# Kernel optimization log

Measured on AMD Instinct MI355X. Metric: run time of the kernel, lower is better.

## Reference

```python
import jax, jax.numpy as jnp
import numpy as np
from jax import lax

TAU = 0.1
LAMBDA_ABCD = 0.5
NUM_ANCHORS = 256
THRESH = 0.6
NEG_INF = -1e30


def sample_features(feat, anchors):
    # feat: [B,C,H,W], anchors: [B,N,2] in [0,1] (u,v). Bilinear, align_corners=False, zeros padding.
    B, C, H, W = feat.shape
    g = anchors * 2.0 - 1.0
    x = ((g[..., 0] + 1.0) * W - 1.0) / 2.0  # [B,N] pixel coords
    y = ((g[..., 1] + 1.0) * H - 1.0) / 2.0
    x0 = jnp.floor(x).astype(jnp.int32); x1 = x0 + 1
    y0 = jnp.floor(y).astype(jnp.int32); y1 = y0 + 1
    wx1 = x - x0.astype(x.dtype); wx0 = 1.0 - wx1
    wy1 = y - y0.astype(y.dtype); wy0 = 1.0 - wy1
    flat = feat.reshape(B, C, H * W)

    def gather(xi, yi):
        valid = ((xi >= 0) & (xi < W) & (yi >= 0) & (yi < H)).astype(feat.dtype)
        idx = jnp.clip(yi, 0, H - 1) * W + jnp.clip(xi, 0, W - 1)  # [B,N]
        v = jnp.take_along_axis(flat, idx[:, None, :], axis=2)  # [B,C,N]
        return v * valid[:, None, :]

    out = (gather(x0, y0) * (wx0 * wy0)[:, None, :]
           + gather(x1, y0) * (wx1 * wy0)[:, None, :]
           + gather(x0, y1) * (wx0 * wy1)[:, None, :]
           + gather(x1, y1) * (wx1 * wy1)[:, None, :])
    return out.transpose(0, 2, 1)  # [B,N,C]


def layer_norm(x, gamma, beta, eps=1e-5):
    mu = x.mean(-1, keepdims=True)
    var = ((x - mu) ** 2).mean(-1, keepdims=True)
    return (x - mu) * lax.rsqrt(var + eps) * gamma + beta


def l2norm(x, eps=1e-12):
    n = jnp.sqrt(jnp.sum(x * x, -1, keepdims=True))
    return x / jnp.maximum(n, eps)


def conv2d(x, w, b, pad):
    y = lax.conv_general_dilated(x, w, (1, 1), pad,
                                 dimension_numbers=('NCHW', 'OIHW', 'NCHW'))
    return y + b[None, :, None, None]


def setup_inputs() -> dict:
    key = jax.random.key(0)
    ks = jax.random.split(key, 12)
    B, Ct, Cs, H, W, P = 16, 1024, 512, 64, 64, 256
    s = lambda k, shp, fan: jax.random.normal(k, shp, jnp.float32) * (1.0 / np.sqrt(fan))
    return {
        'teacher_feat': jax.random.normal(ks[0], (B, Ct, H, W), jnp.float32),
        'student_feat': jax.random.normal(ks[1], (B, Cs, H, W), jnp.float32),
        'conv1_w': s(ks[2], (Ct // 2, Ct, 3, 3), Ct * 9),
        'conv1_b': jnp.zeros((Ct // 2,), jnp.float32),
        'conv2_w': s(ks[3], (1, Ct // 2, 1, 1), Ct // 2),
        'conv2_b': jnp.zeros((1,), jnp.float32),
        't_w': s(ks[4], (Ct, P), Ct), 't_b': jnp.zeros((P,), jnp.float32),
        't_g': jnp.ones((P,), jnp.float32), 't_beta': jnp.zeros((P,), jnp.float32),
        's_w': s(ks[5], (Cs, P), Cs), 's_b': jnp.zeros((P,), jnp.float32),
        's_g': jnp.ones((P,), jnp.float32), 's_beta': jnp.zeros((P,), jnp.float32),
    }


def reference(teacher_feat, student_feat, conv1_w, conv1_b, conv2_w, conv2_b,
              t_w, t_b, t_g, t_beta, s_w, s_b, s_g, s_beta):
    B, Ct, H, W = teacher_feat.shape
    # learnable anchor generator
    h = jax.nn.relu(conv2d(teacher_feat, conv1_w, conv1_b, 'SAME'))
    heatmap = jax.nn.softplus(conv2d(h, conv2_w, conv2_b, 'SAME'))  # [B,1,H,W]
    prob = heatmap.reshape(B, -1)
    prob = prob / (prob.sum(1, keepdims=True) + 1e-6)
    # multinomial without replacement via Gumbel top-k (fixed key -> deterministic)
    u01 = jax.random.uniform(jax.random.key(42), prob.shape, jnp.float32, 1e-8, 1.0)
    gumbel = -jnp.log(-jnp.log(u01))
    idx = lax.top_k(jnp.log(prob + 1e-12) + gumbel, NUM_ANCHORS)[1]  # [B,N]
    ax = (idx % W).astype(jnp.float32) / W
    ay = (idx // W).astype(jnp.float32) / H
    anchors = jnp.stack([ax, ay], -1)  # [B,N,2]

    ft = sample_features(teacher_feat, anchors)  # [B,N,Ct]
    fs = sample_features(student_feat, anchors)  # [B,N,Cs]
    ft = l2norm(layer_norm(jnp.einsum('bnc,cp->bnp', ft, t_w) + t_b, t_g, t_beta))
    fs = l2norm(layer_norm(jnp.einsum('bnc,cp->bnp', fs, s_w) + s_b, s_g, s_beta))

    loss_gafd = jnp.mean((fs - lax.stop_gradient(ft)) ** 2)

    saliency = sample_features(heatmap, anchors)[..., 0]  # [B,N]
    bd = saliency > THRESH * saliency.max(1, keepdims=True)  # [B,N] bool
    non_bd = ~bd

    pos = jnp.sum(fs * ft, -1) / TAU                       # [B,N]
    neg = jnp.einsum('bnc,bmc->bnm', fs, fs) / TAU          # [B,N,N]
    neg = jnp.where(non_bd[:, None, :], neg, NEG_INF)
    logits = jnp.concatenate([pos[..., None], neg], -1)    # [B,N,N+1]
    row_loss = jax.nn.logsumexp(logits, -1) - pos          # [B,N]

    bd_f = bd.astype(jnp.float32)
    cnt = bd_f.sum(1)
    per_b = (row_loss * bd_f).sum(1) / jnp.maximum(cnt, 1.0)
    valid = ((cnt > 0) & (non_bd.sum(1) > 0)).astype(jnp.float32)
    vnum = valid.sum()
    loss_abcd = jnp.where(vnum > 0, (per_b * valid).sum() / jnp.maximum(vnum, 1.0), 0.0)

    total_loss = loss_gafd + LAMBDA_ABCD * loss_abcd
    return total_loss, loss_gafd, loss_abcd, heatmap
```

## Files before the change

### kernel.cpp

```cpp
#include <hip/hip_runtime.h>
#include <stdint.h>


typedef float f32x4 __attribute__((ext_vector_type(4)));
typedef short s16x8 __attribute__((ext_vector_type(8)));

__device__ __forceinline__ unsigned short f2bf(float f) {
  unsigned u = __float_as_uint(f);
  u += 0x7fffu + ((u >> 16) & 1u);
  return (unsigned short)(u >> 16);
}
__device__ __forceinline__ float bf2f(unsigned short h) {
  return __uint_as_float((unsigned)h << 16);
}

__device__ __forceinline__ void gld16(const void* g, void* l) {
  __builtin_amdgcn_global_load_lds(
      (const __attribute__((address_space(1))) void*)g,
      (__attribute__((address_space(3))) void*)l, 16, 0, 0);
}

__device__ __forceinline__ float block_sum(float v, float* l4) {
  for (int m = 32; m; m >>= 1) v += __shfl_xor(v, m, 64);
  int wid = threadIdx.x >> 6;
  if ((threadIdx.x & 63) == 0) l4[wid] = v;
  __syncthreads();
  float r = l4[0] + l4[1] + l4[2] + l4[3];
  __syncthreads();
  return r;
}

__global__ void k_pad_transpose(const float* __restrict__ teacher,
                                unsigned short* __restrict__ tpad) {
  __shared__ __align__(16) unsigned short lds[64 * 65];
  int bid = blockIdx.x;
  int cb = bid & 15, y = (bid >> 4) & 63, b = bid >> 10;
  int t = threadIdx.x;
#pragma unroll
  for (int it = 0; it < 16; ++it) {
    int idx = it * 256 + t;
    int cl = idx >> 6, x = idx & 63;
    float v = teacher[(size_t)(b * 1024 + cb * 64 + cl) * 4096 + y * 64 + x];
    lds[cl * 65 + x] = f2bf(v);
  }
  __syncthreads();
  size_t obase = ((size_t)(b * 66 + y + 1) * 66 + 1) * 1024 + cb * 64;
#pragma unroll
  for (int it = 0; it < 16; ++it) {
    int x = it * 4 + (t >> 6);
    int cl = t & 63;
    tpad[obase + (size_t)x * 1024 + cl] = lds[cl * 65 + x];
  }
  if (y == 0) {
    for (int idx = t; idx < 66 * 64; idx += 256) {
      int col = idx >> 6, cl = idx & 63;
      tpad[((size_t)(b * 66) * 66 + col) * 1024 + cb * 64 + cl] = 0;
    }
  }
  if (y == 63) {
    for (int idx = t; idx < 66 * 64; idx += 256) {
      int col = idx >> 6, cl = idx & 63;
      tpad[((size_t)(b * 66 + 65) * 66 + col) * 1024 + cb * 64 + cl] = 0;
    }
  }
  if (t < 128) {
    int col = (t >= 64) ? 65 : 0;
    int cl = t & 63;
    tpad[((size_t)(b * 66 + y + 1) * 66 + col) * 1024 + cb * 64 + cl] = 0;
  }
}

__global__ void k_wprep(const float* __restrict__ w1,
                        unsigned short* __restrict__ wt) {
  __shared__ float wl[9216];
  int co = blockIdx.x, t = threadIdx.x;
  const float* src = w1 + (size_t)co * 9216;
  for (int i = t; i < 9216; i += 256) wl[i] = src[i];
  __syncthreads();
  for (int i = t; i < 9216; i += 256) {
    int tap = i >> 10;
    int ci = i - (tap << 10);
    int kb = ci >> 6, kc = ci & 63;
    wt[(size_t)tap * 524288 + (size_t)kb * 32768 + co * 64 + kc] = f2bf(wl[ci * 9 + tap]);
  }
}

__global__ void k_wT(const float* __restrict__ w, unsigned short* __restrict__ wT,
                     int K) {
  int e = blockIdx.x * 256 + threadIdx.x;
  int p = e / K, k = e - p * K;
  wT[e] = f2bf(w[(size_t)k * 256 + p]);
}

#define STAGE_A(buf, ts, h) do {                                              \
    int tap_ = (ts) >> 4, kb_ = (ts) & 15;                                    \
    int ky_ = tap_ / 3, kx_ = tap_ - ky_ * 3;                                 \
    unsigned o_ = (unsigned)(((ky_ * 66 + kx_) << 10) + (kb_ << 6));          \
    gld16(tpad + aoff[(h) * 2 + 0] + o_,                                      \
          (char*)(As[buf] + (((h) * 128 + wid * 8) << 6)));                   \
    gld16(tpad + aoff[(h) * 2 + 1] + o_,                                      \
          (char*)(As[buf] + (((h) * 128 + 64 + wid * 8) << 6)));              \
  } while (0)

#define STAGE_B(buf, ts, h) do {                                              \
    int tap_ = (ts) >> 4, kb_ = (ts) & 15;                                    \
    unsigned o_ = (unsigned)((tap_ << 19) + (kb_ << 15));                     \
    gld16(wt + boff[(h) * 2 + 0] + o_,                                        \
          (char*)(Bs[buf] + (((h) * 128 + wid * 8) << 6)));                   \
    gld16(wt + boff[(h) * 2 + 1] + o_,                                        \
          (char*)(Bs[buf] + (((h) * 128 + 64 + wid * 8) << 6)));              \
  } while (0)

#define LDA8(AF, buf, i0)                                                     \
  _Pragma("unroll") for (int i_ = 0; i_ < 4; ++i_)                            \
  _Pragma("unroll") for (int s_ = 0; s_ < 2; ++s_)                            \
    AF[i_][s_] = *(const s16x8*)(const void*)(                                \
        &As[buf][(wm * 128 + ((i0) + i_) * 16 + l15) * 64 +                   \
                 ((s_ * 4 + quad) ^ sw7) * 8]);

#define LDB4(BF, buf, j0)                                                     \
  _Pragma("unroll") for (int j_ = 0; j_ < 2; ++j_)                            \
  _Pragma("unroll") for (int s_ = 0; s_ < 2; ++s_)                            \
    BF[j_][s_] = *(const s16x8*)(const void*)(                                \
        &Bs[buf][(wn * 64 + ((j0) + j_) * 16 + l15) * 64 +                    \
                 ((s_ * 4 + quad) ^ sw7) * 8]);

#define MFMA16(AF, BF, i0, j0)                                                \
  _Pragma("unroll") for (int i_ = 0; i_ < 4; ++i_)                            \
  _Pragma("unroll") for (int j_ = 0; j_ < 2; ++j_)                            \
  _Pragma("unroll") for (int s_ = 0; s_ < 2; ++s_)                            \
    acc[(i0) + i_][(j0) + j_] = __builtin_amdgcn_mfma_f32_16x16x32_bf16(      \
        AF[i_][s_], BF[j_][s_], acc[(i0) + i_][(j0) + j_], 0, 0, 0);

#define PHASE_MID()                                                           \
  __builtin_amdgcn_s_barrier();                                               \
  asm volatile("s_waitcnt lgkmcnt(0)" ::: "memory");                          \
  __builtin_amdgcn_sched_barrier(0);                                          \
  __builtin_amdgcn_s_setprio(1)

#define PHASE_END()                                                           \
  __builtin_amdgcn_s_setprio(0);                                              \
  __builtin_amdgcn_sched_barrier(0);                                          \
  __builtin_amdgcn_s_barrier()

#define PHASE_END_VM()                                                        \
  __builtin_amdgcn_s_setprio(0);                                              \
  __builtin_amdgcn_sched_barrier(0);                                          \
  asm volatile("s_waitcnt vmcnt(4)" ::: "memory");                            \
  __builtin_amdgcn_s_barrier()

__global__ __launch_bounds__(512, 2) void k_conv(
    const unsigned short* __restrict__ tpad, const unsigned short* __restrict__ wt,
    const float* __restrict__ b1, const float* __restrict__ w2,
    float* __restrict__ heat) {
  __shared__ __align__(16) unsigned short As[2][256 * 64];
  __shared__ __align__(16) unsigned short Bs[2][256 * 64];
  int bid = blockIdx.x;
  int swz = (bid & 7) * 64 + (bid >> 3);
  int nt = swz & 1, mt = swz >> 1;
  int m0 = mt * 256, n0 = nt * 256;
  int t = threadIdx.x, wid = t >> 6, lane = t & 63;
  int wm = wid >> 2, wn = wid & 3;
  int quad = lane >> 4, l15 = lane & 15;
  int sw7 = l15 & 7;

  int srcChunk = (t & 7) ^ ((t >> 3) & 7);
  unsigned aoff[4], boff[4];
#pragma unroll
  for (int v = 0; v < 4; ++v) {
    int row = (v >> 1) * 128 + (v & 1) * 64 + (t >> 3);
    int m = m0 + row;
    int b = m >> 12, y = (m >> 6) & 63, x = m & 63;
    aoff[v] = (unsigned)((((b * 66 + y) * 66 + x) << 10) + srcChunk * 8);
    boff[v] = (unsigned)(((n0 + row) << 6) + srcChunk * 8);
  }

  f32x4 acc[8][4];
  const f32x4 fz = {0.f, 0.f, 0.f, 0.f};
#pragma unroll
  for (int i = 0; i < 8; ++i)
#pragma unroll
    for (int j = 0; j < 4; ++j) acc[i][j] = fz;

  STAGE_B(0, 0, 0); STAGE_B(0, 0, 1);
  STAGE_A(0, 0, 0); STAGE_A(0, 0, 1);
  STAGE_B(1, 1, 0); STAGE_B(1, 1, 1);
  asm volatile("s_waitcnt vmcnt(4)" ::: "memory");
  __builtin_amdgcn_s_barrier();

  for (int it2 = 0; it2 < 72; ++it2) {
    int T0 = it2 * 2, T1 = T0 + 1;
    int tsN0 = (T0 + 2 <= 143) ? T0 + 2 : 143;
    int tsN1 = (T1 + 2 <= 143) ? T1 + 2 : 143;
    s16x8 af[4][2], bf01[2][2], bf23[2][2];
    LDA8(af, 0, 0);
    LDB4(bf01, 0, 0);
    STAGE_A(1, T1, 0);
    PHASE_MID();
    MFMA16(af, bf01, 0, 0);
    PHASE_END();

    LDB4(bf23, 0, 2);
    STAGE_A(1, T1, 1);
    PHASE_MID();
    MFMA16(af, bf23, 0, 2);
    PHASE_END();

    LDA8(af, 0, 4);
    STAGE_B(0, tsN0, 0);
    PHASE_MID();
    MFMA16(af, bf01, 4, 0);
    PHASE_END();

    STAGE_B(0, tsN0, 1);
    PHASE_MID();
    MFMA16(af, bf23, 4, 2);
    PHASE_END_VM();

    LDA8(af, 1, 0);
    LDB4(bf01, 1, 0);
    STAGE_A(0, tsN0, 0);
    PHASE_MID();
    MFMA16(af, bf01, 0, 0);
    PHASE_END();

    LDB4(bf23, 1, 2);
    STAGE_A(0, tsN0, 1);
    PHASE_MID();
    MFMA16(af, bf23, 0, 2);
    PHASE_END();

    LDA8(af, 1, 4);
    STAGE_B(1, tsN1, 0);
    PHASE_MID();
    MFMA16(af, bf01, 4, 0);
    PHASE_END();

    STAGE_B(1, tsN1, 1);
    PHASE_MID();
    MFMA16(af, bf23, 4, 2);
    PHASE_END_VM();
  }

  float w2v[4], b1v[4];
#pragma unroll
  for (int j = 0; j < 4; ++j) {
    int co = n0 + wn * 64 + j * 16 + l15;
    w2v[j] = w2[co];
    b1v[j] = b1[co];
  }
#pragma unroll
  for (int i = 0; i < 8; ++i) {
#pragma unroll
    for (int r = 0; r < 4; ++r) {
      float part = 0.f;
#pragma unroll
      for (int j = 0; j < 4; ++j) {
        float v = acc[i][j][r] + b1v[j];
        v = fmaxf(v, 0.f);
        part += v * w2v[j];
      }
#pragma unroll
      for (int msk = 1; msk < 16; msk <<= 1) part += __shfl_xor(part, msk, 64);
      if (l15 == 0) atomicAdd(&heat[m0 + wm * 128 + i * 16 + quad * 4 + r], part);
    }
  }
}

__device__ __forceinline__ unsigned rotl32(unsigned x, int d) {
  return (x << d) | (x >> (32 - d));
}
__device__ unsigned threefry_bits(unsigned lo) {
  const unsigned k0 = 0u, k1 = 42u;
  const unsigned k2 = 0x1BD11BDAu ^ k0 ^ k1;
  unsigned x0 = 0u + k0, x1 = lo + k1;
#define TF_R4(a, bq, c, d)                                \
  x0 += x1; x1 = rotl32(x1, a); x1 ^= x0;                 \
  x0 += x1; x1 = rotl32(x1, bq); x1 ^= x0;                \
  x0 += x1; x1 = rotl32(x1, c); x1 ^= x0;                 \
  x0 += x1; x1 = rotl32(x1, d); x1 ^= x0;
  TF_R4(13, 15, 26, 6)  x0 += k1; x1 += k2 + 1u;
  TF_R4(17, 29, 16, 24) x0 += k2; x1 += k0 + 2u;
  TF_R4(13, 15, 26, 6)  x0 += k0; x1 += k1 + 3u;
  TF_R4(17, 29, 16, 24) x0 += k1; x1 += k2 + 4u;
  TF_R4(13, 15, 26, 6)  x0 += k2; x1 += k0 + 5u;
#undef TF_R4
  return x0 ^ x1;
}

__global__ void k_heat2score(const float* __restrict__ heat, const float* __restrict__ b2p,
                             float* __restrict__ out_hm, float* __restrict__ hm,
                             float* __restrict__ scores) {
  __shared__ float l4[4];
  int b = blockIdx.x, t = threadIdx.x;
  float b2 = b2p[0];
  float hv[16];
  float lsum = 0.f;
#pragma unroll
  for (int j = 0; j < 16; ++j) {
    int e = j * 256 + t;
    float x = heat[b * 4096 + e] + b2;
    float sp = fmaxf(x, 0.f) + log1pf(expf(-fabsf(x)));
    hv[j] = sp;
    lsum += sp;
  }
  float S = block_sum(lsum, l4);
  float denom = S + 1e-6f;
#pragma unroll
  for (int j = 0; j < 16; ++j) {
    int e = j * 256 + t;
    float sp = hv[j];
    out_hm[b * 4096 + e] = sp;
    hm[b * 4096 + e] = sp;
    float lp = logf(sp / denom + 1e-12f);
    unsigned bits = threefry_bits((unsigned)(b * 4096 + e));
    float u01 = __uint_as_float((bits >> 9) | 0x3f800000u) - 1.0f;
    float u = fmaxf(1e-8f, u01 * (1.0f - 1e-8f) + 1e-8f);
    float gum = -logf(-logf(u));
    scores[b * 4096 + e] = lp + gum;
  }
}

__global__ void k_topk(const float* __restrict__ scores, int* __restrict__ idx_sel) {
  __shared__ unsigned keys[4096];
  __shared__ unsigned hist[256];
  __shared__ unsigned suf[256];
  __shared__ unsigned sel[2];
  __shared__ int wpos;
  int b = blockIdx.x, t = threadIdx.x;
#pragma unroll
  for (int j = 0; j < 16; ++j) {
    unsigned u = __float_as_uint(scores[b * 4096 + j * 256 + t]);
    u = (u >> 31) ? ~u : (u | 0x80000000u);
    keys[j * 256 + t] = u;
  }
  if (t == 0) wpos = 0;
  unsigned prefix = 0, hmask = 0, r = 256;
  for (int pass = 0; pass < 4; ++pass) {
    int shift = 24 - 8 * pass;
    hist[t] = 0;
    __syncthreads();
#pragma unroll
    for (int j = 0; j < 16; ++j) {
      unsigned u = keys[j * 256 + t];
      if ((u & hmask) == prefix) atomicAdd(&hist[(u >> shift) & 255u], 1u);
    }
    __syncthreads();
    suf[t] = hist[t];
    __syncthreads();
    for (int off = 1; off < 256; off <<= 1) {
      unsigned v = (t + off < 256) ? suf[t + off] : 0u;
      __syncthreads();
      suf[t] += v;
      __syncthreads();
    }
    unsigned above = (t < 255) ? suf[t + 1] : 0u;
    if (suf[t] >= r && above < r) {
      sel[0] = (unsigned)t;
      sel[1] = above;
    }
    __syncthreads();
    prefix |= sel[0] << shift;
    hmask |= 0xFFu << shift;
    r -= sel[1];
    __syncthreads();
  }
#pragma unroll
  for (int j = 0; j < 16; ++j) {
    int e = j * 256 + t;
    if (keys[e] > prefix) {
      int s = atomicAdd(&wpos, 1);
      idx_sel[b * 256 + s] = e;
    }
  }
  __syncthreads();
#pragma unroll
  for (int j = 0; j < 16; ++j) {
    int e = j * 256 + t;
    if (keys[e] == prefix) {
      int s = atomicAdd(&wpos, 1);
      if (s < 256) idx_sel[b * 256 + s] = e;
    }
  }
}

__global__ void k_gather_t(const unsigned short* __restrict__ tpad,
                           const int* __restrict__ idx_sel,
                           unsigned short* __restrict__ ftb) {
  int bn = blockIdx.x;
  int b = bn >> 8;
  int idx = idx_sel[bn];
  int px = idx & 63, py = idx >> 6;
  const unsigned short* base = tpad + ((size_t)(b * 66 + py) * 66 + px) * 1024;
  for (int c = threadIdx.x; c < 1024; c += 256) {
    float v = bf2f(base[c]) + bf2f(base[c + 1024]) +
              bf2f(base[c + 66 * 1024]) + bf2f(base[c + 67 * 1024]);
    ftb[(size_t)bn * 1024 + c] = f2bf(0.25f * v);
  }
}

__global__ void k_gather_s(const float* __restrict__ student,
                           const int* __restrict__ idx_sel,
                           unsigned short* __restrict__ fsbT) {
  __shared__ float plane[4096];
  int blk = blockIdx.x;
  int b = blk >> 9, c = blk & 511;
  int t = threadIdx.x;
  const float4* g4 = (const float4*)(student + ((size_t)b * 512 + c) * 4096);
  float4* p4 = (float4*)plane;
  for (int i = t; i < 1024; i += 256) p4[i] = g4[i];
  __syncthreads();
  int idx = idx_sel[b * 256 + t];
  int px = idx & 63, py = idx >> 6;
  float v = 0.f;
  if (py > 0) {
    if (px > 0) v += plane[(py - 1) * 64 + px - 1];
    v += plane[(py - 1) * 64 + px];
  }
  if (px > 0) v += plane[py * 64 + px - 1];
  v += plane[py * 64 + px];
  fsbT[((size_t)b * 512 + c) * 256 + t] = f2bf(0.25f * v);
}

__global__ void k_fsb_tr(const unsigned short* __restrict__ fsbT,
                         unsigned short* __restrict__ fsb) {
  __shared__ unsigned short tile[64][65];
  int blk = blockIdx.x;
  int b = blk >> 5, ct = (blk >> 2) & 7, nt = blk & 3;
  int t = threadIdx.x;
#pragma unroll
  for (int it = 0; it < 16; ++it) {
    int e = it * 256 + t;
    int cl = e >> 6, n = e & 63;
    tile[cl][n] = fsbT[((size_t)(b * 512 + ct * 64 + cl)) * 256 + nt * 64 + n];
  }
  __syncthreads();
#pragma unroll
  for (int it = 0; it < 16; ++it) {
    int e = it * 256 + t;
    int n = e >> 6, cl = e & 63;
    fsb[((size_t)(b * 256 + nt * 64 + n)) * 512 + ct * 64 + cl] = tile[cl][n];
  }
}

__global__ __launch_bounds__(256) void k_proj(
    const unsigned short* __restrict__ A, const unsigned short* __restrict__ Wt,
    int K, float* __restrict__ outp) {
  __shared__ __align__(16) unsigned short As[128 * 64];
  __shared__ __align__(16) unsigned short Bs[128 * 64];
  int bid = blockIdx.x;
  int nt = bid & 1, mt = bid >> 1;
  int m0 = mt * 128, n0 = nt * 128;
  int t = threadIdx.x, wid = t >> 6, lane = t & 63;
  int wm = wid & 1, wn = wid >> 1;
  int quad = lane >> 4, l15 = lane & 15;

  f32x4 acc[4][4];
  const f32x4 fz = {0.f, 0.f, 0.f, 0.f};
#pragma unroll
  for (int i = 0; i < 4; ++i)
#pragma unroll
    for (int j = 0; j < 4; ++j) acc[i][j] = fz;

  int row4[4];
#pragma unroll
  for (int jj = 0; jj < 4; ++jj) row4[jj] = (wid * 4 + jj) * 8 + (lane >> 3);
  int kcol = (lane & 7) * 8;

  int nkb = K >> 6;
  for (int kb = 0; kb < nkb; ++kb) {
#pragma unroll
    for (int jj = 0; jj < 4; ++jj) {
      gld16(A + (size_t)(m0 + row4[jj]) * K + kb * 64 + kcol,
            (char*)As + (wid * 4 + jj) * 1024);
      gld16(Wt + (size_t)(n0 + row4[jj]) * K + kb * 64 + kcol,
            (char*)Bs + (wid * 4 + jj) * 1024);
    }
    __syncthreads();
#pragma unroll
    for (int s = 0; s < 2; ++s) {
      s16x8 af[4], bf[4];
#pragma unroll
      for (int i = 0; i < 4; ++i) {
        af[i] = *(const s16x8*)(const void*)(As + (wm * 64 + i * 16 + l15) * 64 + s * 32 + quad * 8);
        bf[i] = *(const s16x8*)(const void*)(Bs + (wn * 64 + i * 16 + l15) * 64 + s * 32 + quad * 8);
      }
#pragma unroll
      for (int i = 0; i < 4; ++i)
#pragma unroll
        for (int j = 0; j < 4; ++j)
          acc[i][j] = __builtin_amdgcn_mfma_f32_16x16x32_bf16(af[i], bf[j], acc[i][j], 0, 0, 0);
    }
    __syncthreads();
  }
#pragma unroll
  for (int i = 0; i < 4; ++i)
#pragma unroll
    for (int j = 0; j < 4; ++j)
#pragma unroll
      for (int r = 0; r < 4; ++r) {
        int m = m0 + wm * 64 + i * 16 + quad * 4 + r;
        int p = n0 + wn * 64 + j * 16 + l15;
        outp[(size_t)m * 256 + p] = acc[i][j][r];
      }
}

__global__ void k_ln(const float* __restrict__ projp, const float* __restrict__ bias,
                     const float* __restrict__ g, const float* __restrict__ beta,
                     float* __restrict__ outf, unsigned short* __restrict__ outb) {
  __shared__ float l4[4];
  int row = blockIdx.x, t = threadIdx.x;
  float x = projp[(size_t)row * 256 + t] + bias[t];
  float s1 = block_sum(x, l4);
  float mu = s1 * (1.f / 256.f);
  float d = x - mu;
  float s2 = block_sum(d * d, l4);
  float rstd = rsqrtf(s2 * (1.f / 256.f) + 1e-5f);
  float xn = d * rstd * g[t] + beta[t];
  float ss = block_sum(xn * xn, l4);
  float o = xn / fmaxf(sqrtf(ss), 1e-12f);
  outf[(size_t)row * 256 + t] = o;
  if (outb) outb[(size_t)row * 256 + t] = f2bf(o);
}

__global__ void k_sal(const float* __restrict__ hm, const int* __restrict__ idx_sel,
                      int* __restrict__ bd, int* __restrict__ cnt, int* __restrict__ nbc) {
  __shared__ float l4[4];
  int b = blockIdx.x, t = threadIdx.x;
  int idx = idx_sel[b * 256 + t];
  int px = idx & 63, py = idx >> 6;
  const float* hb = hm + b * 4096;
  float v = 0.f;
  if (py > 0) {
    if (px > 0) v += hb[(py - 1) * 64 + px - 1];
    v += hb[(py - 1) * 64 + px];
  }
  if (px > 0) v += hb[py * 64 + px - 1];
  v += hb[py * 64 + px];
  float sal = 0.25f * v;
  float mx = sal;
  for (int m = 32; m; m >>= 1) mx = fmaxf(mx, __shfl_xor(mx, m, 64));
  if ((t & 63) == 0) l4[t >> 6] = mx;
  __syncthreads();
  mx = fmaxf(fmaxf(l4[0], l4[1]), fmaxf(l4[2], l4[3]));
  __syncthreads();
  int bdv = sal > 0.6f * mx ? 1 : 0;
  bd[b * 256 + t] = bdv;
  float c = block_sum((float)bdv, l4);
  if (t == 0) {
    cnt[b] = (int)c;
    nbc[b] = 256 - (int)c;
  }
}

__global__ void k_pos_gafd(const float* __restrict__ fsn, const float* __restrict__ ftn,
                           float* __restrict__ pos, float* __restrict__ gsum) {
  __shared__ float l4[4];
  int row = blockIdx.x, t = threadIdx.x;
  float a = fsn[(size_t)row * 256 + t];
  float bt = ftn[(size_t)row * 256 + t];
  float sdot = block_sum(a * bt, l4);
  if (t == 0) pos[row] = sdot * 10.f;
  float d = a - bt;
  float ssq = block_sum(d * d, l4);
  if (t == 0) atomicAdd(gsum, ssq);
}

__global__ __launch_bounds__(256) void k_abcd_rows(
    const unsigned short* __restrict__ fsnb, const int* __restrict__ bd,
    const float* __restrict__ pos, float* __restrict__ rowloss) {
  __shared__ __align__(16) unsigned short Ab[64 * 64];
  __shared__ __align__(16) unsigned short Bb[256 * 64];
  __shared__ float mrg[64][4][2];
  int b = blockIdx.x >> 2, nb = blockIdx.x & 3;
  int n0 = nb * 64;
  int t = threadIdx.x, w = t >> 6, lane = t & 63, quad = lane >> 4, l15 = lane & 15;
  f32x4 acc[4][4];
  const f32x4 fz = {0.f, 0.f, 0.f, 0.f};
#pragma unroll
  for (int i = 0; i < 4; ++i)
#pragma unroll
    for (int j = 0; j < 4; ++j) acc[i][j] = fz;
  const unsigned short* fb = fsnb + (size_t)b * 256 * 256;

  for (int kc = 0; kc < 4; ++kc) {
    {
      int r = t >> 2, cc = (t & 3) * 16;
      const uint4* s = (const uint4*)(const void*)(fb + (size_t)(n0 + r) * 256 + kc * 64 + cc);
      *(uint4*)(void*)(Ab + r * 64 + cc) = s[0];
      *(uint4*)(void*)(Ab + r * 64 + cc + 8) = s[1];
    }
#pragma unroll
    for (int it = 0; it < 4; ++it) {
      int m = it * 64 + (t >> 2), cc = (t & 3) * 16;
      const uint4* s = (const uint4*)(const void*)(fb + (size_t)m * 256 + kc * 64 + cc);
      *(uint4*)(void*)(Bb + m * 64 + cc) = s[0];
      *(uint4*)(void*)(Bb + m * 64 + cc + 8) = s[1];
    }
    __syncthreads();
#pragma unroll
    for (int s = 0; s < 2; ++s) {
      s16x8 af[4], bf[4];
#pragma unroll
      for (int i = 0; i < 4; ++i) {
        af[i] = *(const s16x8*)(const void*)(Ab + (i * 16 + l15) * 64 + s * 32 + quad * 8);
        bf[i] = *(const s16x8*)(const void*)(Bb + (w * 64 + i * 16 + l15) * 64 + s * 32 + quad * 8);
      }
#pragma unroll
      for (int i = 0; i < 4; ++i)
#pragma unroll
        for (int j = 0; j < 4; ++j)
          acc[i][j] = __builtin_amdgcn_mfma_f32_16x16x32_bf16(af[i], bf[j], acc[i][j], 0, 0, 0);
    }
    __syncthreads();
  }

  int nbmask[4];
#pragma unroll
  for (int j = 0; j < 4; ++j) nbmask[j] = bd[b * 256 + w * 64 + j * 16 + l15];
#pragma unroll
  for (int i = 0; i < 4; ++i) {
#pragma unroll
    for (int r = 0; r < 4; ++r) {
      float mxv = -1e30f, se = 0.f;
#pragma unroll
      for (int j = 0; j < 4; ++j) {
        float v = nbmask[j] ? -1e30f : (acc[i][j][r] / 0.1f);
        if (v > mxv) {
          se = se * expf(mxv - v) + 1.f;
          mxv = v;
        } else {
          se += expf(v - mxv);
        }
      }
#pragma unroll
      for (int msk = 1; msk < 16; msk <<= 1) {
        float omx = __shfl_xor(mxv, msk, 64);
        float ose = __shfl_xor(se, msk, 64);
        float nm = fmaxf(mxv, omx);
        se = se * expf(mxv - nm) + ose * expf(omx - nm);
        mxv = nm;
      }
      if (l15 == 0) {
        mrg[i * 16 + quad * 4 + r][w][0] = mxv;
        mrg[i * 16 + quad * 4 + r][w][1] = se;
      }
    }
  }
  __syncthreads();
  if (t < 64) {
    float MX = -1e30f, SE = 0.f;
    for (int ww = 0; ww < 4; ++ww) {
      float omx = mrg[t][ww][0], ose = mrg[t][ww][1];
      float nm = fmaxf(MX, omx);
      SE = SE * expf(MX - nm) + ose * expf(omx - nm);
      MX = nm;
    }
    float p = pos[b * 256 + n0 + t];
    float nm = fmaxf(MX, p);
    float se2 = SE * expf(MX - nm) + expf(p - nm);
    rowloss[b * 256 + n0 + t] = nm + logf(se2) - p;
  }
}

__global__ void k_final(const float* __restrict__ gsum, const float* __restrict__ rowloss,
                        const int* __restrict__ bd, const int* __restrict__ cnt,
                        const int* __restrict__ nbc, float* __restrict__ out) {
  __shared__ float l4[4];
  int t = threadIdx.x;
  float abcd_acc = 0.f, vnum = 0.f;
  for (int b = 0; b < 16; ++b) {
    float c = bd[b * 256 + t] ? rowloss[b * 256 + t] : 0.f;
    float s = block_sum(c, l4);
    if (t == 0) {
      float cb = (float)cnt[b];
      float per = s / fmaxf(cb, 1.f);
      if (cnt[b] > 0 && nbc[b] > 0) {
        abcd_acc += per;
        vnum += 1.f;
      }
    }
  }
  if (t == 0) {
    float gafd = gsum[0] / 1048576.f;
    float abcd = vnum > 0.f ? abcd_acc / fmaxf(vnum, 1.f) : 0.f;
    out[0] = gafd + 0.5f * abcd;
    out[1] = gafd;
    out[2] = abcd;
  }
}

static constexpr size_t OFF_TPAD = 0;
static constexpr size_t TPAD_BYTES = (size_t)16 * 66 * 66 * 1024 * 2;
static constexpr size_t OFF_WT = OFF_TPAD + TPAD_BYTES;
static constexpr size_t WT_BYTES = (size_t)9 * 16 * 512 * 64 * 2;
static constexpr size_t OFF_HEAT = OFF_WT + WT_BYTES;
static constexpr size_t OFF_GSUM = OFF_HEAT + 262144;
static constexpr size_t OFF_HM = OFF_GSUM + 256;
static constexpr size_t OFF_SC = OFF_HM + 262144;
static constexpr size_t OFF_IDX = OFF_SC + 262144;
static constexpr size_t OFF_FTB = OFF_IDX + 16384;
static constexpr size_t OFF_FSB = OFF_FTB + (size_t)4096 * 1024 * 2;
static constexpr size_t OFF_FSBT = OFF_FSB + (size_t)4096 * 512 * 2;
static constexpr size_t OFF_WTT = OFF_FSBT + (size_t)4096 * 512 * 2;
static constexpr size_t OFF_WTS = OFF_WTT + (size_t)256 * 1024 * 2;
static constexpr size_t OFF_PRT = OFF_WTS + (size_t)256 * 512 * 2;
static constexpr size_t OFF_PRS = OFF_PRT + (size_t)4096 * 256 * 4;
static constexpr size_t OFF_FTN = OFF_PRS + (size_t)4096 * 256 * 4;
static constexpr size_t OFF_FSN = OFF_FTN + (size_t)4096 * 256 * 4;
static constexpr size_t OFF_FSNB = OFF_FSN + (size_t)4096 * 256 * 4;
static constexpr size_t OFF_POS = OFF_FSNB + (size_t)4096 * 256 * 2;
static constexpr size_t OFF_BD = OFF_POS + 16384;
static constexpr size_t OFF_CNT = OFF_BD + 16384;
static constexpr size_t OFF_NBC = OFF_CNT + 64;
static constexpr size_t OFF_RL = OFF_NBC + 64;

extern "C" void kernel_launch(void* const* d_in, const int* in_sizes, int n_in,
                              void* d_out, int out_size, void* d_ws, size_t ws_size,
                              hipStream_t stream) {
  const float* teacher = (const float*)d_in[0];
  const float* student = (const float*)d_in[1];
  const float* w1 = (const float*)d_in[2];
  const float* b1 = (const float*)d_in[3];
  const float* w2 = (const float*)d_in[4];
  const float* b2 = (const float*)d_in[5];
  const float* t_w = (const float*)d_in[6];
  const float* t_b = (const float*)d_in[7];
  const float* t_g = (const float*)d_in[8];
  const float* t_be = (const float*)d_in[9];
  const float* s_w = (const float*)d_in[10];
  const float* s_b = (const float*)d_in[11];
  const float* s_g = (const float*)d_in[12];
  const float* s_be = (const float*)d_in[13];
  float* out = (float*)d_out;

  char* ws = (char*)d_ws;
  unsigned short* tpad = (unsigned short*)(ws + OFF_TPAD);
  unsigned short* wt = (unsigned short*)(ws + OFF_WT);
  float* heat = (float*)(ws + OFF_HEAT);
  float* gsum = (float*)(ws + OFF_GSUM);
  float* hm = (float*)(ws + OFF_HM);
  float* scores = (float*)(ws + OFF_SC);
  int* idx_sel = (int*)(ws + OFF_IDX);
  unsigned short* ftb = (unsigned short*)(ws + OFF_FTB);
  unsigned short* fsb = (unsigned short*)(ws + OFF_FSB);
  unsigned short* fsbT = (unsigned short*)(ws + OFF_FSBT);
  unsigned short* wTt = (unsigned short*)(ws + OFF_WTT);
  unsigned short* wTs = (unsigned short*)(ws + OFF_WTS);
  float* projt = (float*)(ws + OFF_PRT);
  float* projs = (float*)(ws + OFF_PRS);
  float* ftn = (float*)(ws + OFF_FTN);
  float* fsn = (float*)(ws + OFF_FSN);
  unsigned short* fsnb = (unsigned short*)(ws + OFF_FSNB);
  float* pos = (float*)(ws + OFF_POS);
  int* bd = (int*)(ws + OFF_BD);
  int* cnt = (int*)(ws + OFF_CNT);
  int* nbc = (int*)(ws + OFF_NBC);
  float* rowloss = (float*)(ws + OFF_RL);

  hipMemsetAsync(ws + OFF_HEAT, 0, 262144 + 256, stream);

  k_pad_transpose<<<16384, 256, 0, stream>>>(teacher, tpad);
  k_wprep<<<512, 256, 0, stream>>>(w1, wt);
  k_wT<<<1024, 256, 0, stream>>>(t_w, wTt, 1024);
  k_wT<<<512, 256, 0, stream>>>(s_w, wTs, 512);
  k_conv<<<512, 512, 0, stream>>>(tpad, wt, b1, w2, heat);
  k_heat2score<<<16, 256, 0, stream>>>(heat, b2, out + 3, hm, scores);
  k_topk<<<16, 256, 0, stream>>>(scores, idx_sel);
  k_gather_t<<<4096, 256, 0, stream>>>(tpad, idx_sel, ftb);
  k_gather_s<<<8192, 256, 0, stream>>>(student, idx_sel, fsbT);
  k_fsb_tr<<<512, 256, 0, stream>>>(fsbT, fsb);
  k_proj<<<64, 256, 0, stream>>>(ftb, wTt, 1024, projt);
  k_proj<<<64, 256, 0, stream>>>(fsb, wTs, 512, projs);
  k_ln<<<4096, 256, 0, stream>>>(projt, t_b, t_g, t_be, ftn, (unsigned short*)nullptr);
  k_ln<<<4096, 256, 0, stream>>>(projs, s_b, s_g, s_be, fsn, fsnb);
  k_sal<<<16, 256, 0, stream>>>(hm, idx_sel, bd, cnt, nbc);
  k_pos_gafd<<<4096, 256, 0, stream>>>(fsn, ftn, pos, gsum);
  k_abcd_rows<<<64, 256, 0, stream>>>(fsnb, bd, pos, rowloss);
  k_final<<<1, 256, 0, stream>>>(gsum, rowloss, bd, cnt, nbc, out);
}
```

Measured before the change: 1.194 ms.

## Fuse small kernels, vectorize transpose/gather, and reorder conv LDS loads

Several kernels are merged: the three weight-prep kernels become one launch, score/topk/saliency become one per-batch kernel that keeps the heatmap in LDS, the two projection GEMMs share one launch, and the student layernorm is fused with the pos/GAFD reduction. The pad-transpose and teacher gather now use 16-byte vector loads and stores. In the conv main loop, LDS fragment loads are issued earlier so they overlap with the preceding MFMAs. Together these cut launch overhead and intermediate global round-trips, at the cost of more LDS use and register pressure in the fused kernels.

```diff
diff --git a/kernel.cpp b/kernel.cpp
--- a/kernel.cpp
+++ b/kernel.cpp
@@ -37,19 +37,25 @@
   int cb = bid & 15, y = (bid >> 4) & 63, b = bid >> 10;
   int t = threadIdx.x;
 #pragma unroll
-  for (int it = 0; it < 16; ++it) {
+  for (int it = 0; it < 4; ++it) {
     int idx = it * 256 + t;
-    int cl = idx >> 6, x = idx & 63;
-    float v = teacher[(size_t)(b * 1024 + cb * 64 + cl) * 4096 + y * 64 + x];
-    lds[cl * 65 + x] = f2bf(v);
+    int cl = idx >> 4, x4 = (idx & 15) * 4;
+    float4 v = *(const float4*)&teacher[(size_t)(b * 1024 + cb * 64 + cl) * 4096 + y * 64 + x4];
+    lds[cl * 65 + x4 + 0] = f2bf(v.x);
+    lds[cl * 65 + x4 + 1] = f2bf(v.y);
+    lds[cl * 65 + x4 + 2] = f2bf(v.z);
+    lds[cl * 65 + x4 + 3] = f2bf(v.w);
   }
   __syncthreads();
   size_t obase = ((size_t)(b * 66 + y + 1) * 66 + 1) * 1024 + cb * 64;
 #pragma unroll
-  for (int it = 0; it < 16; ++it) {
-    int x = it * 4 + (t >> 6);
-    int cl = t & 63;
-    tpad[obase + (size_t)x * 1024 + cl] = lds[cl * 65 + x];
+  for (int it = 0; it < 2; ++it) {
+    int wi = it * 256 + t;
+    int x = wi >> 3, c0 = (wi & 7) * 8;
+    s16x8 v;
+#pragma unroll
+    for (int k2 = 0; k2 < 8; ++k2) v[k2] = (short)lds[(c0 + k2) * 65 + x];
+    *(s16x8*)(void*)&tpad[obase + (size_t)x * 1024 + c0] = v;
   }
   if (y == 0) {
     for (int idx = t; idx < 66 * 64; idx += 256) {
@@ -70,26 +76,32 @@
   }
 }
 
-__global__ void k_wprep(const float* __restrict__ w1,
-                        unsigned short* __restrict__ wt) {
-  __shared__ float wl[9216];
-  int co = blockIdx.x, t = threadIdx.x;
-  const float* src = w1 + (size_t)co * 9216;
-  for (int i = t; i < 9216; i += 256) wl[i] = src[i];
-  __syncthreads();
-  for (int i = t; i < 9216; i += 256) {
-    int tap = i >> 10;
-    int ci = i - (tap << 10);
-    int kb = ci >> 6, kc = ci & 63;
-    wt[(size_t)tap * 524288 + (size_t)kb * 32768 + co * 64 + kc] = f2bf(wl[ci * 9 + tap]);
-  }
-}
-
-__global__ void k_wT(const float* __restrict__ w, unsigned short* __restrict__ wT,
-                     int K) {
-  int e = blockIdx.x * 256 + threadIdx.x;
-  int p = e / K, k = e - p * K;
-  wT[e] = f2bf(w[(size_t)k * 256 + p]);
+__global__ void k_wprep_all(const float* __restrict__ w1,
+                            unsigned short* __restrict__ wt,
+                            const float* __restrict__ tw, unsigned short* __restrict__ wTt,
+                            const float* __restrict__ sw, unsigned short* __restrict__ wTs) {
+  int blk = blockIdx.x, t = threadIdx.x;
+  if (blk < 512) {
+    __shared__ float wl[9216];
+    int co = blk;
+    const float* src = w1 + (size_t)co * 9216;
+    for (int i = t; i < 9216; i += 256) wl[i] = src[i];
+    __syncthreads();
+    for (int i = t; i < 9216; i += 256) {
+      int tap = i >> 10;
+      int ci = i - (tap << 10);
+      int kb = ci >> 6, kc = ci & 63;
+      wt[(size_t)tap * 524288 + (size_t)kb * 32768 + co * 64 + kc] = f2bf(wl[ci * 9 + tap]);
+    }
+  } else if (blk < 1536) {
+    int e = (blk - 512) * 256 + t;
+    int p = e >> 10, k = e & 1023;
+    wTt[e] = f2bf(tw[(size_t)k * 256 + p]);
+  } else {
+    int e = (blk - 1536) * 256 + t;
+    int p = e >> 9, k = e & 511;
+    wTs[e] = f2bf(sw[(size_t)k * 256 + p]);
+  }
 }
 
 #define STAGE_A(buf, ts, h) do {                                              \
@@ -189,54 +201,54 @@
   __builtin_amdgcn_s_barrier();
 
   for (int it2 = 0; it2 < 72; ++it2) {
-    int T0 = it2 * 2, T1 = T0 + 1;
-    int tsN0 = (T0 + 2 <= 143) ? T0 + 2 : 143;
-    int tsN1 = (T1 + 2 <= 143) ? T1 + 2 : 143;
+    int T1 = it2 * 2 + 1;
+    int tsA = (T1 + 1 <= 143) ? T1 + 1 : 143;
+    int tsB = (T1 + 2 <= 143) ? T1 + 2 : 143;
     s16x8 af[4][2], bf01[2][2], bf23[2][2];
     LDA8(af, 0, 0);
     LDB4(bf01, 0, 0);
     STAGE_A(1, T1, 0);
     PHASE_MID();
     MFMA16(af, bf01, 0, 0);
+    LDB4(bf23, 0, 2);
     PHASE_END();
 
-    LDB4(bf23, 0, 2);
     STAGE_A(1, T1, 1);
     PHASE_MID();
     MFMA16(af, bf23, 0, 2);
+    LDA8(af, 0, 4);
     PHASE_END();
 
-    LDA8(af, 0, 4);
-    STAGE_B(0, tsN0, 0);
+    STAGE_B(0, tsA, 0);
     PHASE_MID();
     MFMA16(af, bf01, 4, 0);
     PHASE_END();
 
-    STAGE_B(0, tsN0, 1);
+    STAGE_B(0, tsA, 1);
     PHASE_MID();
     MFMA16(af, bf23, 4, 2);
     PHASE_END_VM();
 
     LDA8(af, 1, 0);
     LDB4(bf01, 1, 0);
-    STAGE_A(0, tsN0, 0);
+    STAGE_A(0, tsA, 0);
     PHASE_MID();
     MFMA16(af, bf01, 0, 0);
+    LDB4(bf23, 1, 2);
     PHASE_END();
 
-    LDB4(bf23, 1, 2);
-    STAGE_A(0, tsN0, 1);
+    STAGE_A(0, tsA, 1);
     PHASE_MID();
     MFMA16(af, bf23, 0, 2);
+    LDA8(af, 1, 4);
     PHASE_END();
 
-    LDA8(af, 1, 4);
-    STAGE_B(1, tsN1, 0);
+    STAGE_B(1, tsB, 0);
     PHASE_MID();
     MFMA16(af, bf01, 4, 0);
     PHASE_END();
 
-    STAGE_B(1, tsN1, 1);
+    STAGE_B(1, tsB, 1);
     PHASE_MID();
     MFMA16(af, bf23, 4, 2);
     PHASE_END_VM();
@@ -288,20 +300,29 @@
   return x0 ^ x1;
 }
 
-__global__ void k_heat2score(const float* __restrict__ heat, const float* __restrict__ b2p,
-                             float* __restrict__ out_hm, float* __restrict__ hm,
-                             float* __restrict__ scores) {
+__global__ void k_score_topk_sal(const float* __restrict__ heat,
+                                 const float* __restrict__ b2p,
+                                 float* __restrict__ out_hm,
+                                 int* __restrict__ idx_sel,
+                                 int* __restrict__ bd, int* __restrict__ cnt,
+                                 int* __restrict__ nbc) {
+  __shared__ float hmp[4096];
+  __shared__ unsigned keys[4096];
+  __shared__ unsigned hist[256];
+  __shared__ unsigned suf[256];
+  __shared__ unsigned sel[2];
+  __shared__ int wpos;
+  __shared__ int idxl[256];
   __shared__ float l4[4];
   int b = blockIdx.x, t = threadIdx.x;
   float b2 = b2p[0];
-  float hv[16];
   float lsum = 0.f;
 #pragma unroll
   for (int j = 0; j < 16; ++j) {
     int e = j * 256 + t;
     float x = heat[b * 4096 + e] + b2;
     float sp = fmaxf(x, 0.f) + log1pf(expf(-fabsf(x)));
-    hv[j] = sp;
+    hmp[e] = sp;
     lsum += sp;
   }
   float S = block_sum(lsum, l4);
@@ -309,30 +330,17 @@
 #pragma unroll
   for (int j = 0; j < 16; ++j) {
     int e = j * 256 + t;
-    float sp = hv[j];
+    float sp = hmp[e];
     out_hm[b * 4096 + e] = sp;
-    hm[b * 4096 + e] = sp;
     float lp = logf(sp / denom + 1e-12f);
     unsigned bits = threefry_bits((unsigned)(b * 4096 + e));
     float u01 = __uint_as_float((bits >> 9) | 0x3f800000u) - 1.0f;
     float u = fmaxf(1e-8f, u01 * (1.0f - 1e-8f) + 1e-8f);
     float gum = -logf(-logf(u));
-    scores[b * 4096 + e] = lp + gum;
-  }
-}
-
-__global__ void k_topk(const float* __restrict__ scores, int* __restrict__ idx_sel) {
-  __shared__ unsigned keys[4096];
-  __shared__ unsigned hist[256];
-  __shared__ unsigned suf[256];
-  __shared__ unsigned sel[2];
-  __shared__ int wpos;
-  int b = blockIdx.x, t = threadIdx.x;
-#pragma unroll
-  for (int j = 0; j < 16; ++j) {
-    unsigned u = __float_as_uint(scores[b * 4096 + j * 256 + t]);
-    u = (u >> 31) ? ~u : (u | 0x80000000u);
-    keys[j * 256 + t] = u;
+    float sc = lp + gum;
+    unsigned uu = __float_as_uint(sc);
+    uu = (uu >> 31) ? ~uu : (uu | 0x80000000u);
+    keys[e] = uu;
   }
   if (t == 0) wpos = 0;
   unsigned prefix = 0, hmask = 0, r = 256;
@@ -371,6 +379,7 @@
     if (keys[e] > prefix) {
       int s = atomicAdd(&wpos, 1);
       idx_sel[b * 256 + s] = e;
+      idxl[s] = e;
     }
   }
   __syncthreads();
@@ -379,24 +388,60 @@
     int e = j * 256 + t;
     if (keys[e] == prefix) {
       int s = atomicAdd(&wpos, 1);
-      if (s < 256) idx_sel[b * 256 + s] = e;
-    }
+      if (s < 256) {
+        idx_sel[b * 256 + s] = e;
+        idxl[s] = e;
+      }
+    }
+  }
+  __syncthreads();
+  int idx = idxl[t];
+  int px = idx & 63, py = idx >> 6;
+  float v = 0.f;
+  if (py > 0) {
+    if (px > 0) v += hmp[(py - 1) * 64 + px - 1];
+    v += hmp[(py - 1) * 64 + px];
+  }
+  if (px > 0) v += hmp[py * 64 + px - 1];
+  v += hmp[py * 64 + px];
+  float sal = 0.25f * v;
+  float mx = sal;
+  for (int m = 32; m; m >>= 1) mx = fmaxf(mx, __shfl_xor(mx, m, 64));
+  if ((t & 63) == 0) l4[t >> 6] = mx;
+  __syncthreads();
+  mx = fmaxf(fmaxf(l4[0], l4[1]), fmaxf(l4[2], l4[3]));
+  __syncthreads();
+  int bdv = sal > 0.6f * mx ? 1 : 0;
+  bd[b * 256 + t] = bdv;
+  float c = block_sum((float)bdv, l4);
+  if (t == 0) {
+    cnt[b] = (int)c;
+    nbc[b] = 256 - (int)c;
   }
 }
 
 __global__ void k_gather_t(const unsigned short* __restrict__ tpad,
                            const int* __restrict__ idx_sel,
                            unsigned short* __restrict__ ftb) {
-  int bn = blockIdx.x;
+  int t = threadIdx.x;
+  int bn = blockIdx.x * 2 + (t >> 7);
+  int tt = t & 127;
   int b = bn >> 8;
   int idx = idx_sel[bn];
   int px = idx & 63, py = idx >> 6;
-  const unsigned short* base = tpad + ((size_t)(b * 66 + py) * 66 + px) * 1024;
-  for (int c = threadIdx.x; c < 1024; c += 256) {
-    float v = bf2f(base[c]) + bf2f(base[c + 1024]) +
-              bf2f(base[c + 66 * 1024]) + bf2f(base[c + 67 * 1024]);
-    ftb[(size_t)bn * 1024 + c] = f2bf(0.25f * v);
-  }
+  const unsigned short* base = tpad + ((size_t)(b * 66 + py) * 66 + px) * 1024 + tt * 8;
+  s16x8 r0 = *(const s16x8*)(const void*)(base);
+  s16x8 r1 = *(const s16x8*)(const void*)(base + 1024);
+  s16x8 r2 = *(const s16x8*)(const void*)(base + 66 * 1024);
+  s16x8 r3 = *(const s16x8*)(const void*)(base + 67 * 1024);
+  s16x8 o;
+#pragma unroll
+  for (int k = 0; k < 8; ++k) {
+    float v = bf2f((unsigned short)r0[k]) + bf2f((unsigned short)r1[k]) +
+              bf2f((unsigned short)r2[k]) + bf2f((unsigned short)r3[k]);
+    o[k] = (short)f2bf(0.25f * v);
+  }
+  *(s16x8*)(void*)&ftb[(size_t)bn * 1024 + tt * 8] = o;
 }
 
 __global__ void k_gather_s(const float* __restrict__ student,
@@ -443,12 +488,19 @@
   }
 }
 
-__global__ __launch_bounds__(256) void k_proj(
-    const unsigned short* __restrict__ A, const unsigned short* __restrict__ Wt,
-    int K, float* __restrict__ outp) {
-  __shared__ __align__(16) unsigned short As[128 * 64];
-  __shared__ __align__(16) unsigned short Bs[128 * 64];
-  int bid = blockIdx.x;
+__global__ __launch_bounds__(256) void k_proj_both(
+    const unsigned short* __restrict__ At, const unsigned short* __restrict__ Wtt,
+    const unsigned short* __restrict__ Asrc, const unsigned short* __restrict__ Wts,
+    float* __restrict__ outt, float* __restrict__ outs) {
+  __shared__ __align__(16) unsigned short Al[128 * 64];
+  __shared__ __align__(16) unsigned short Bl[128 * 64];
+  int g = blockIdx.x;
+  const unsigned short* A;
+  const unsigned short* Wt;
+  float* outp;
+  int K, bid;
+  if (g < 64) { A = At; Wt = Wtt; outp = outt; K = 1024; bid = g; }
+  else        { A = Asrc; Wt = Wts; outp = outs; K = 512; bid = g - 64; }
   int nt = bid & 1, mt = bid >> 1;
   int m0 = mt * 128, n0 = nt * 128;
   int t = threadIdx.x, wid = t >> 6, lane = t & 63;
@@ -472,9 +524,9 @@
 #pragma unroll
     for (int jj = 0; jj < 4; ++jj) {
       gld16(A + (size_t)(m0 + row4[jj]) * K + kb * 64 + kcol,
-            (char*)As + (wid * 4 + jj) * 1024);
+            (char*)Al + (wid * 4 + jj) * 1024);
       gld16(Wt + (size_t)(n0 + row4[jj]) * K + kb * 64 + kcol,
-            (char*)Bs + (wid * 4 + jj) * 1024);
+            (char*)Bl + (wid * 4 + jj) * 1024);
     }
     __syncthreads();
 #pragma unroll
@@ -482,8 +534,8 @@
       s16x8 af[4], bf[4];
 #pragma unroll
       for (int i = 0; i < 4; ++i) {
-        af[i] = *(const s16x8*)(const void*)(As + (wm * 64 + i * 16 + l15) * 64 + s * 32 + quad * 8);
-        bf[i] = *(const s16x8*)(const void*)(Bs + (wn * 64 + i * 16 + l15) * 64 + s * 32 + quad * 8);
+        af[i] = *(const s16x8*)(const void*)(Al + (wm * 64 + i * 16 + l15) * 64 + s * 32 + quad * 8);
+        bf[i] = *(const s16x8*)(const void*)(Bl + (wn * 64 + i * 16 + l15) * 64 + s * 32 + quad * 8);
       }
 #pragma unroll
       for (int i = 0; i < 4; ++i)
@@ -507,7 +559,7 @@
 
 __global__ void k_ln(const float* __restrict__ projp, const float* __restrict__ bias,
                      const float* __restrict__ g, const float* __restrict__ beta,
-                     float* __restrict__ outf, unsigned short* __restrict__ outb) {
+                     float* __restrict__ outf) {
   __shared__ float l4[4];
   int row = blockIdx.x, t = threadIdx.x;
   float x = projp[(size_t)row * 256 + t] + bias[t];
@@ -520,49 +572,31 @@
   float ss = block_sum(xn * xn, l4);
   float o = xn / fmaxf(sqrtf(ss), 1e-12f);
   outf[(size_t)row * 256 + t] = o;
-  if (outb) outb[(size_t)row * 256 + t] = f2bf(o);
-}
-
-__global__ void k_sal(const float* __restrict__ hm, const int* __restrict__ idx_sel,
-                      int* __restrict__ bd, int* __restrict__ cnt, int* __restrict__ nbc) {
-  __shared__ float l4[4];
-  int b = blockIdx.x, t = threadIdx.x;
-  int idx = idx_sel[b * 256 + t];
-  int px = idx & 63, py = idx >> 6;
-  const float* hb = hm + b * 4096;
-  float v = 0.f;
-  if (py > 0) {
-    if (px > 0) v += hb[(py - 1) * 64 + px - 1];
-    v += hb[(py - 1) * 64 + px];
-  }
-  if (px > 0) v += hb[py * 64 + px - 1];
-  v += hb[py * 64 + px];
-  float sal = 0.25f * v;
-  float mx = sal;
-  for (int m = 32; m; m >>= 1) mx = fmaxf(mx, __shfl_xor(mx, m, 64));
-  if ((t & 63) == 0) l4[t >> 6] = mx;
-  __syncthreads();
-  mx = fmaxf(fmaxf(l4[0], l4[1]), fmaxf(l4[2], l4[3]));
-  __syncthreads();
-  int bdv = sal > 0.6f * mx ? 1 : 0;
-  bd[b * 256 + t] = bdv;
-  float c = block_sum((float)bdv, l4);
-  if (t == 0) {
-    cnt[b] = (int)c;
-    nbc[b] = 256 - (int)c;
-  }
-}
-
-__global__ void k_pos_gafd(const float* __restrict__ fsn, const float* __restrict__ ftn,
+}
+
+__global__ void k_ln_s_pos(const float* __restrict__ projp, const float* __restrict__ bias,
+                           const float* __restrict__ g, const float* __restrict__ beta,
+                           const float* __restrict__ ftn,
+                           float* __restrict__ outf, unsigned short* __restrict__ outb,
                            float* __restrict__ pos, float* __restrict__ gsum) {
   __shared__ float l4[4];
   int row = blockIdx.x, t = threadIdx.x;
-  float a = fsn[(size_t)row * 256 + t];
+  float x = projp[(size_t)row * 256 + t] + bias[t];
+  float s1 = block_sum(x, l4);
+  float mu = s1 * (1.f / 256.f);
+  float d = x - mu;
+  float s2 = block_sum(d * d, l4);
+  float rstd = rsqrtf(s2 * (1.f / 256.f) + 1e-5f);
+  float xn = d * rstd * g[t] + beta[t];
+  float ss = block_sum(xn * xn, l4);
+  float o = xn / fmaxf(sqrtf(ss), 1e-12f);
+  outf[(size_t)row * 256 + t] = o;
+  outb[(size_t)row * 256 + t] = f2bf(o);
   float bt = ftn[(size_t)row * 256 + t];
-  float sdot = block_sum(a * bt, l4);
+  float sdot = block_sum(o * bt, l4);
   if (t == 0) pos[row] = sdot * 10.f;
-  float d = a - bt;
-  float ssq = block_sum(d * d, l4);
+  float dd = o - bt;
+  float ssq = block_sum(dd * dd, l4);
   if (t == 0) atomicAdd(gsum, ssq);
 }
 
@@ -739,8 +773,6 @@
   unsigned short* wt = (unsigned short*)(ws + OFF_WT);
   float* heat = (float*)(ws + OFF_HEAT);
   float* gsum = (float*)(ws + OFF_GSUM);
-  float* hm = (float*)(ws + OFF_HM);
-  float* scores = (float*)(ws + OFF_SC);
   int* idx_sel = (int*)(ws + OFF_IDX);
   unsigned short* ftb = (unsigned short*)(ws + OFF_FTB);
   unsigned short* fsb = (unsigned short*)(ws + OFF_FSB);
@@ -761,21 +793,15 @@
   hipMemsetAsync(ws + OFF_HEAT, 0, 262144 + 256, stream);
 
   k_pad_transpose<<<16384, 256, 0, stream>>>(teacher, tpad);
-  k_wprep<<<512, 256, 0, stream>>>(w1, wt);
-  k_wT<<<1024, 256, 0, stream>>>(t_w, wTt, 1024);
-  k_wT<<<512, 256, 0, stream>>>(s_w, wTs, 512);
+  k_wprep_all<<<2048, 256, 0, stream>>>(w1, wt, t_w, wTt, s_w, wTs);
   k_conv<<<512, 512, 0, stream>>>(tpad, wt, b1, w2, heat);
-  k_heat2score<<<16, 256, 0, stream>>>(heat, b2, out + 3, hm, scores);
-  k_topk<<<16, 256, 0, stream>>>(scores, idx_sel);
-  k_gather_t<<<4096, 256, 0, stream>>>(tpad, idx_sel, ftb);
+  k_score_topk_sal<<<16, 256, 0, stream>>>(heat, b2, out + 3, idx_sel, bd, cnt, nbc);
+  k_gather_t<<<2048, 256, 0, stream>>>(tpad, idx_sel, ftb);
   k_gather_s<<<8192, 256, 0, stream>>>(student, idx_sel, fsbT);
   k_fsb_tr<<<512, 256, 0, stream>>>(fsbT, fsb);
-  k_proj<<<64, 256, 0, stream>>>(ftb, wTt, 1024, projt);
-  k_proj<<<64, 256, 0, stream>>>(fsb, wTs, 512, projs);
-  k_ln<<<4096, 256, 0, stream>>>(projt, t_b, t_g, t_be, ftn, (unsigned short*)nullptr);
-  k_ln<<<4096, 256, 0, stream>>>(projs, s_b, s_g, s_be, fsn, fsnb);
-  k_sal<<<16, 256, 0, stream>>>(hm, idx_sel, bd, cnt, nbc);
-  k_pos_gafd<<<4096, 256, 0, stream>>>(fsn, ftn, pos, gsum);
+  k_proj_both<<<128, 256, 0, stream>>>(ftb, wTt, fsb, wTs, projt, projs);
+  k_ln<<<4096, 256, 0, stream>>>(projt, t_b, t_g, t_be, ftn);
+  k_ln_s_pos<<<4096, 256, 0, stream>>>(projs, s_b, s_g, s_be, ftn, fsn, fsnb, pos, gsum);
   k_abcd_rows<<<64, 256, 0, stream>>>(fsnb, bd, pos, rowloss);
   k_final<<<1, 256, 0, stream>>>(gsum, rowloss, bd, cnt, nbc, out);
 }
```

Result: faster. 1.144 ms (-4.2%).
